# Kernel optimization log

Hardware: AMD Instinct MI355X
Metric: run time of the kernel (lower is better)

The kernel has to match this reference:

```python
import math
import jax, jax.numpy as jnp
import numpy as np

DIM = 4096
N_HEADS = 32
N_KV_HEADS = 8
HEAD_DIM = DIM // N_HEADS          # 128
N_REP = N_HEADS // N_KV_HEADS      # 4
B, T = 2, 2048
MAX_SEQ = 2048
ROPE_THETA = 500000.0


def _rope_tables(seq_len, head_dim, theta):
    inv = 1.0 / (theta ** (np.arange(0, head_dim, 2, dtype=np.float32) / head_dim))
    t = np.arange(seq_len, dtype=np.float32)
    ang = np.outer(t, inv)                      # [T, head_dim/2]
    return jnp.asarray(np.cos(ang)), jnp.asarray(np.sin(ang))


def setup_inputs() -> dict:
    key = jax.random.key(0)
    ks = jax.random.split(key, 6)
    scale = 0.02
    x = jax.random.normal(ks[0], (B, T, DIM), dtype=jnp.float32)
    wq = jax.random.normal(ks[1], (N_HEADS * HEAD_DIM, DIM), dtype=jnp.float32) * scale
    wk = jax.random.normal(ks[2], (N_KV_HEADS * HEAD_DIM, DIM), dtype=jnp.float32) * scale
    wv = jax.random.normal(ks[3], (N_KV_HEADS * HEAD_DIM, DIM), dtype=jnp.float32) * scale
    wo = jax.random.normal(ks[4], (DIM, N_HEADS * HEAD_DIM), dtype=jnp.float32) * scale
    freqs_cos, freqs_sin = _rope_tables(T, HEAD_DIM, ROPE_THETA)
    cache_k = jnp.zeros((B, MAX_SEQ, N_KV_HEADS, HEAD_DIM), dtype=jnp.float32)
    cache_v = jnp.zeros((B, MAX_SEQ, N_KV_HEADS, HEAD_DIM), dtype=jnp.float32)
    mask = jnp.zeros((T, T), dtype=jnp.float32)  # NOTE: unused by the original forward
    return {"x": x, "wq": wq, "wk": wk, "wv": wv, "wo": wo,
            "freqs_cos": freqs_cos, "freqs_sin": freqs_sin,
            "cache_k": cache_k, "cache_v": cache_v,
            "mask": mask, "start_pos": 0}


def _apply_rope(t, cos, sin):
    # t: [B, T, H, hd]; even/odd interleaved pairs form complex numbers
    tr = t.reshape(*t.shape[:-1], HEAD_DIM // 2, 2)
    xr, xi = tr[..., 0], tr[..., 1]
    c = cos[None, :, None, :]
    s = sin[None, :, None, :]
    out_r = xr * c - xi * s
    out_i = xr * s + xi * c
    return jnp.stack([out_r, out_i], axis=-1).reshape(t.shape)


def reference(x, wq, wk, wv, wo, freqs_cos, freqs_sin, cache_k, cache_v, mask, start_pos):
    Bx, Tx, _ = x.shape
    q = (x @ wq.T).reshape(Bx, Tx, N_HEADS, HEAD_DIM)
    k = (x @ wk.T).reshape(Bx, Tx, N_KV_HEADS, HEAD_DIM)
    v = (x @ wv.T).reshape(Bx, Tx, N_KV_HEADS, HEAD_DIM)

    q = _apply_rope(q, freqs_cos, freqs_sin)
    k = _apply_rope(k, freqs_cos, freqs_sin)

    # KV-cache append (start_pos is a static Python int)
    cache_k = jax.lax.dynamic_update_slice(cache_k, k, (0, start_pos, 0, 0))
    cache_v = jax.lax.dynamic_update_slice(cache_v, v, (0, start_pos, 0, 0))
    S = start_pos + Tx

    # GQA expansion via torch-style .repeat (tiling: head h -> kv head h % n_kv)
    keys = jnp.tile(cache_k[:, :S], (1, 1, N_REP, 1))    # [B, S, H, hd]
    values = jnp.tile(cache_v[:, :S], (1, 1, N_REP, 1))  # [B, S, H, hd]

    scores = jnp.einsum('bthd,bshd->bhts', q, keys) / math.sqrt(HEAD_DIM)
    # NOTE: the original forward never adds `mask` — faithful unmasked softmax
    probs = jax.nn.softmax(scores, axis=-1)
    ctx = jnp.einsum('bhts,bshd->bthd', probs, values).reshape(Bx, Tx, N_HEADS * HEAD_DIM)
    return ctx @ wo.T
```

## Files before the change

### kernel.cpp

```cpp
#include <hip/hip_runtime.h>
#include <hip/hip_bf16.h>
#include <cstdint>


typedef short bf16x8 __attribute__((ext_vector_type(8)));
typedef float f32x4  __attribute__((ext_vector_type(4)));

__device__ __forceinline__ float b2f(unsigned short h) {
  union { uint32_t u; float f; } v; v.u = ((uint32_t)h) << 16; return v.f;
}
__device__ __forceinline__ unsigned short f2b(float f) {
  union { float f; uint32_t u; } v; v.f = f;
  uint32_t r = (v.u + 0x7FFFu + ((v.u >> 16) & 1u)) >> 16;
  return (unsigned short)r;
}

#define GLDS16(gp, lp)                                                        \
  __builtin_amdgcn_global_load_lds(                                           \
      (const __attribute__((address_space(1))) unsigned int*)(gp),            \
      (__attribute__((address_space(3))) unsigned int*)(lp), 16, 0, 0)

__global__ __launch_bounds__(256) void cast_f32_bf16(
    const float* __restrict__ in, unsigned short* __restrict__ out, int n4) {
  int i = blockIdx.x * 256 + threadIdx.x;
  if (i < n4) {
    float4 v = ((const float4*)in)[i];
    ushort4 o;
    o.x = f2b(v.x); o.y = f2b(v.y); o.z = f2b(v.z); o.w = f2b(v.w);
    ((ushort4*)out)[i] = o;
  }
}

__device__ __forceinline__ void stout(float* p, float v) { *p = v; }
__device__ __forceinline__ void stout(unsigned short* p, float v) { *p = f2b(v); }

template <typename OUT>
__global__ __launch_bounds__(256, 2) void gemm_bt(
    const unsigned short* __restrict__ A, const unsigned short* __restrict__ B,
    OUT* __restrict__ C, int M, int N, int K) {
  __shared__ __align__(16) unsigned short As[128][64];
  __shared__ __align__(16) unsigned short Bs[128][64];

  const int tid  = threadIdx.x;
  const int lane = tid & 63;
  const int wave = tid >> 6;
  const int col  = lane & 15;
  const int quad = lane >> 4;
  const int bm = blockIdx.y * 128;
  const int bn = blockIdx.x * 128;
  const int wm = (wave & 1) * 64;
  const int wn = (wave >> 1) * 64;

  f32x4 acc[4][4];
#pragma unroll
  for (int i = 0; i < 4; ++i)
#pragma unroll
    for (int j = 0; j < 4; ++j) acc[i][j] = (f32x4){0.f, 0.f, 0.f, 0.f};

  const int srow0  = tid >> 3;
  const int gchunk = (tid & 7) ^ ((tid >> 3) & 7);
  const unsigned short* Ag = A + (size_t)(bm + srow0) * K + gchunk * 8;
  const unsigned short* Bg = B + (size_t)(bn + srow0) * K + gchunk * 8;
  unsigned short* Al = &As[0][0] + tid * 8;
  unsigned short* Bl = &Bs[0][0] + tid * 8;

  for (int k0 = 0; k0 < K; k0 += 64) {
    __syncthreads();
#pragma unroll
    for (int r = 0; r < 4; ++r) {
      GLDS16(Ag + k0 + (size_t)r * 32 * K, Al + r * 2048);
      GLDS16(Bg + k0 + (size_t)r * 32 * K, Bl + r * 2048);
    }
    __syncthreads();
#pragma unroll
    for (int ks = 0; ks < 2; ++ks) {
      bf16x8 a[4], b[4];
      const int slot = ((ks * 4 + quad) ^ (col & 7)) * 8;
#pragma unroll
      for (int i = 0; i < 4; ++i)
        a[i] = *(const bf16x8*)&As[wm + i * 16 + col][slot];
#pragma unroll
      for (int j = 0; j < 4; ++j)
        b[j] = *(const bf16x8*)&Bs[wn + j * 16 + col][slot];
#pragma unroll
      for (int i = 0; i < 4; ++i)
#pragma unroll
        for (int j = 0; j < 4; ++j)
          acc[i][j] = __builtin_amdgcn_mfma_f32_16x16x32_bf16(a[i], b[j],
                                                              acc[i][j], 0, 0, 0);
    }
  }

#pragma unroll
  for (int i = 0; i < 4; ++i) {
    int row = bm + wm + i * 16 + quad * 4;
#pragma unroll
    for (int j = 0; j < 4; ++j) {
      int cc = bn + wn + j * 16 + col;
#pragma unroll
      for (int r2 = 0; r2 < 4; ++r2)
        stout(C + (size_t)(row + r2) * N + cc, acc[i][j][r2]);
    }
  }
}

__global__ __launch_bounds__(256) void rope_qk(
    unsigned short* __restrict__ qkv, const float* __restrict__ cosT,
    const float* __restrict__ sinT) {
  int idx = blockIdx.x * 256 + threadIdx.x;
  int m = idx / 2560;
  int p = idx - m * 2560;
  int head = p >> 6, i = p & 63;
  int t = m & 2047;
  unsigned short* ptr = qkv + (size_t)m * 6144 + head * 128 + i * 2;
  ushort2 xy = *(const ushort2*)ptr;
  float x = b2f(xy.x), y = b2f(xy.y);
  float c = cosT[t * 64 + i], s = sinT[t * 64 + i];
  ushort2 o;
  o.x = f2b(x * c - y * s);
  o.y = f2b(x * s + y * c);
  *(ushort2*)ptr = o;
}

__global__ __launch_bounds__(256) void transpose_v(
    const unsigned short* __restrict__ qkv, unsigned short* __restrict__ vt) {
  __shared__ unsigned short tile[64][72];
  int b = blockIdx.z >> 3, kvh = blockIdx.z & 7;
  int s0 = blockIdx.x * 64, d0 = blockIdx.y * 64;
  int tc = threadIdx.x & 63, tr = threadIdx.x >> 6;
#pragma unroll
  for (int r = 0; r < 16; ++r) {
    int row = r * 4 + tr;
    tile[row][tc] =
        qkv[(size_t)(b * 2048 + s0 + row) * 6144 + 5120 + kvh * 128 + d0 + tc];
  }
  __syncthreads();
#pragma unroll
  for (int r = 0; r < 16; ++r) {
    int drow = r * 4 + tr;
    vt[(size_t)((b * 8 + kvh) * 128 + d0 + drow) * 2048 + s0 + tc] =
        tile[tc][drow];
  }
}

__global__ __launch_bounds__(256, 2) void attn(
    const unsigned short* __restrict__ qkv, const unsigned short* __restrict__ vt,
    unsigned short* __restrict__ ctx) {
  constexpr int T = 2048, LD = 6144;
  const int qt = blockIdx.x, h = blockIdx.y, b = blockIdx.z;
  const int kvh = h & 7;
  const int tid = threadIdx.x, lane = tid & 63, wave = tid >> 6;
  const int col = lane & 15, quad = lane >> 4;

  __shared__ __align__(1024) char smem[49152];
  auto Qs = (unsigned short(*)[128][8])smem;
  auto Ks = (unsigned short(*)[64][8])smem;
  auto Vs = (unsigned short(*)[128][8])(smem + 16384);
  auto Ps = (unsigned short(*)[128][8])(smem + 32768);

  {
    const int row = tid & 127, kc0 = tid >> 7;
    const unsigned short* g =
        qkv + (size_t)(b * T + qt * 128 + row) * LD + h * 128 + kc0 * 8;
    unsigned short* l = &Qs[kc0][row][0];
#pragma unroll
    for (int r = 0; r < 8; ++r) GLDS16(g + r * 16, l + r * 2048);
  }
  __syncthreads();

  bf16x8 qf[2][4];
#pragma unroll
  for (int mi = 0; mi < 2; ++mi)
#pragma unroll
    for (int ks = 0; ks < 4; ++ks)
      qf[mi][ks] = *(const bf16x8*)&Qs[ks * 4 + quad][wave * 32 + mi * 16 + col][0];

  float mrow[2][4], lrow[2][4];
  f32x4 oacc[2][8];
#pragma unroll
  for (int mi = 0; mi < 2; ++mi)
#pragma unroll
    for (int r = 0; r < 4; ++r) { mrow[mi][r] = -1e30f; lrow[mi][r] = 0.f; }
#pragma unroll
  for (int mi = 0; mi < 2; ++mi)
#pragma unroll
    for (int d = 0; d < 8; ++d) oacc[mi][d] = (f32x4){0.f, 0.f, 0.f, 0.f};

  const float scale = 0.08838834764831845f;
  const float l2e = 1.4426950408889634f;

  for (int s0 = 0; s0 < T; s0 += 64) {
    __syncthreads();
    {
      const int srow = tid & 63, kc0 = tid >> 6;
      const unsigned short* g =
          qkv + (size_t)(b * T + s0 + srow) * LD + 4096 + kvh * 128 + kc0 * 8;
      unsigned short* l = &Ks[kc0][srow][0];
#pragma unroll
      for (int r = 0; r < 4; ++r) GLDS16(g + r * 32, l + r * 2048);
      const int drow = tid & 127, sc0 = tid >> 7;
      const unsigned short* gv =
          vt + (size_t)((b * 8 + kvh) * 128 + drow) * T + s0 + sc0 * 8;
      unsigned short* lv = &Vs[sc0][drow][0];
#pragma unroll
      for (int r = 0; r < 4; ++r) GLDS16(gv + r * 16, lv + r * 2048);
    }
    __syncthreads();

    f32x4 sacc[2][4];
#pragma unroll
    for (int mi = 0; mi < 2; ++mi)
#pragma unroll
      for (int j = 0; j < 4; ++j) sacc[mi][j] = (f32x4){0.f, 0.f, 0.f, 0.f};
#pragma unroll
    for (int ks = 0; ks < 4; ++ks) {
      bf16x8 bk[4];
#pragma unroll
      for (int j = 0; j < 4; ++j)
        bk[j] = *(const bf16x8*)&Ks[ks * 4 + quad][j * 16 + col][0];
#pragma unroll
      for (int mi = 0; mi < 2; ++mi)
#pragma unroll
        for (int j = 0; j < 4; ++j)
          sacc[mi][j] = __builtin_amdgcn_mfma_f32_16x16x32_bf16(
              qf[mi][ks], bk[j], sacc[mi][j], 0, 0, 0);
    }

#pragma unroll
    for (int mi = 0; mi < 2; ++mi) {
#pragma unroll
      for (int r = 0; r < 4; ++r) {
        float mx = sacc[mi][0][r];
#pragma unroll
        for (int j = 1; j < 4; ++j) mx = fmaxf(mx, sacc[mi][j][r]);
        mx = fmaxf(mx, __shfl_xor(mx, 1));
        mx = fmaxf(mx, __shfl_xor(mx, 2));
        mx = fmaxf(mx, __shfl_xor(mx, 4));
        mx = fmaxf(mx, __shfl_xor(mx, 8));
        mx *= scale;
        float mold = mrow[mi][r];
        float mnew = fmaxf(mold, mx);
        float alpha = exp2f((mold - mnew) * l2e);
        mrow[mi][r] = mnew;
        float rsum = 0.f;
#pragma unroll
        for (int j = 0; j < 4; ++j) {
          float pv = exp2f((sacc[mi][j][r] * scale - mnew) * l2e);
          sacc[mi][j][r] = pv;
          rsum += pv;
        }
        rsum += __shfl_xor(rsum, 1);
        rsum += __shfl_xor(rsum, 2);
        rsum += __shfl_xor(rsum, 4);
        rsum += __shfl_xor(rsum, 8);
        lrow[mi][r] = lrow[mi][r] * alpha + rsum;
#pragma unroll
        for (int d = 0; d < 8; ++d) oacc[mi][d][r] *= alpha;
        int prow = wave * 32 + mi * 16 + quad * 4 + r;
#pragma unroll
        for (int j = 0; j < 4; ++j) {
          int sc = (j * 16 + col) >> 3;
          Ps[sc][prow][col & 7] = f2b(sacc[mi][j][r]);
        }
      }
    }

#pragma unroll
    for (int ks = 0; ks < 2; ++ks) {
      bf16x8 ap[2];
#pragma unroll
      for (int mi = 0; mi < 2; ++mi)
        ap[mi] = *(const bf16x8*)&Ps[ks * 4 + quad][wave * 32 + mi * 16 + col][0];
#pragma unroll
      for (int di = 0; di < 8; ++di) {
        bf16x8 bv = *(const bf16x8*)&Vs[ks * 4 + quad][di * 16 + col][0];
#pragma unroll
        for (int mi = 0; mi < 2; ++mi)
          oacc[mi][di] = __builtin_amdgcn_mfma_f32_16x16x32_bf16(
              ap[mi], bv, oacc[mi][di], 0, 0, 0);
      }
    }
  }

#pragma unroll
  for (int mi = 0; mi < 2; ++mi) {
#pragma unroll
    for (int r = 0; r < 4; ++r) {
      float inv = 1.0f / lrow[mi][r];
      int row = qt * 128 + wave * 32 + mi * 16 + quad * 4 + r;
#pragma unroll
      for (int di = 0; di < 8; ++di)
        ctx[(size_t)(b * T + row) * 4096 + h * 128 + di * 16 + col] =
            f2b(oacc[mi][di][r] * inv);
    }
  }
}

extern "C" void kernel_launch(void* const* d_in, const int* in_sizes, int n_in,
                              void* d_out, int out_size, void* d_ws,
                              size_t ws_size, hipStream_t stream) {
  const float* x  = (const float*)d_in[0];
  const float* wq = (const float*)d_in[1];
  const float* wk = (const float*)d_in[2];
  const float* wv = (const float*)d_in[3];
  const float* wo = (const float*)d_in[4];
  const float* fc = (const float*)d_in[5];
  const float* fs = (const float*)d_in[6];
  float* out = (float*)d_out;

  char* ws = (char*)d_ws;
  unsigned short* xb  = (unsigned short*)(ws);
  unsigned short* wb  = (unsigned short*)(ws + 33554432);
  unsigned short* qkv = (unsigned short*)(ws + 33554432 + 50331648);
  unsigned short* vtp = (unsigned short*)(ws + 33554432 + 50331648 + 50331648);

  cast_f32_bf16<<<16384, 256, 0, stream>>>(x, xb, 4194304);
  cast_f32_bf16<<<16384, 256, 0, stream>>>(wq, wb, 4194304);
  cast_f32_bf16<<<4096, 256, 0, stream>>>(wk, wb + 16777216, 1048576);
  cast_f32_bf16<<<4096, 256, 0, stream>>>(wv, wb + 20971520, 1048576);

  dim3 g1(48, 32);
  gemm_bt<unsigned short><<<g1, 256, 0, stream>>>(xb, wb, qkv, 4096, 6144, 4096);

  cast_f32_bf16<<<16384, 256, 0, stream>>>(wo, wb, 4194304);

  rope_qk<<<40960, 256, 0, stream>>>(qkv, fc, fs);

  dim3 g2(32, 2, 16);
  transpose_v<<<g2, 256, 0, stream>>>(qkv, vtp);

  dim3 g3(16, 32, 2);
  attn<<<g3, 256, 0, stream>>>(qkv, vtp, xb);

  dim3 g4(32, 32);
  gemm_bt<float><<<g4, 256, 0, stream>>>(xb, wb, out, 4096, 4096, 4096);
}
```

Before: 929.7 us.

## Transpose attention MFMAs so query rows live per lane, with swizzled K/V LDS

The QK^T and PV MFMAs now take K/V as the A operand and Q/P as B, so each lane holds one query's scores across its accumulator registers. The row max and row sum then need only two cross-quad shuffles instead of four per row, and P is written to LDS as packed 4-element vectors. K and V tiles are stored row-major with an XOR swizzle on 16-byte chunks to avoid LDS bank conflicts, and the P buffer is padded to 72 columns. Shared memory grows slightly, which may affect occupancy at two blocks per CU, and the output stores become scattered 2-byte writes.

```diff
diff --git a/kernel.cpp b/kernel.cpp
--- a/kernel.cpp
+++ b/kernel.cpp
@@ -152,11 +152,11 @@
   const int tid = threadIdx.x, lane = tid & 63, wave = tid >> 6;
   const int col = lane & 15, quad = lane >> 4;
 
-  __shared__ __align__(1024) char smem[49152];
+  __shared__ __align__(1024) char smem[51200];
   auto Qs = (unsigned short(*)[128][8])smem;
-  auto Ks = (unsigned short(*)[64][8])smem;
-  auto Vs = (unsigned short(*)[128][8])(smem + 16384);
-  auto Ps = (unsigned short(*)[128][8])(smem + 32768);
+  auto Ks = (unsigned short(*)[128])smem;
+  auto Vs = (unsigned short(*)[64])(smem + 16384);
+  auto Ps = (unsigned short(*)[72])(smem + 32768);
 
   {
     const int row = tid & 127, kc0 = tid >> 7;
@@ -175,12 +175,10 @@
     for (int ks = 0; ks < 4; ++ks)
       qf[mi][ks] = *(const bf16x8*)&Qs[ks * 4 + quad][wave * 32 + mi * 16 + col][0];
 
-  float mrow[2][4], lrow[2][4];
+  float mrow[2], lrow[2];
   f32x4 oacc[2][8];
 #pragma unroll
-  for (int mi = 0; mi < 2; ++mi)
-#pragma unroll
-    for (int r = 0; r < 4; ++r) { mrow[mi][r] = -1e30f; lrow[mi][r] = 0.f; }
+  for (int mi = 0; mi < 2; ++mi) { mrow[mi] = -1e30f; lrow[mi] = 0.f; }
 #pragma unroll
   for (int mi = 0; mi < 2; ++mi)
 #pragma unroll
@@ -188,22 +186,27 @@
 
   const float scale = 0.08838834764831845f;
   const float l2e = 1.4426950408889634f;
+
+  const int krow0 = tid >> 4;
+  const int kgch  = (tid & 15) ^ ((tid >> 4) & 15);
+  const int vrow0 = tid >> 3;
+  const int vgch  = (tid & 7) ^ ((tid >> 3) & 7);
+  unsigned short* Klin = &Ks[0][0] + tid * 8;
+  unsigned short* Vlin = &Vs[0][0] + tid * 8;
 
   for (int s0 = 0; s0 < T; s0 += 64) {
     __syncthreads();
     {
-      const int srow = tid & 63, kc0 = tid >> 6;
       const unsigned short* g =
-          qkv + (size_t)(b * T + s0 + srow) * LD + 4096 + kvh * 128 + kc0 * 8;
-      unsigned short* l = &Ks[kc0][srow][0];
-#pragma unroll
-      for (int r = 0; r < 4; ++r) GLDS16(g + r * 32, l + r * 2048);
-      const int drow = tid & 127, sc0 = tid >> 7;
+          qkv + (size_t)(b * T + s0 + krow0) * LD + 4096 + kvh * 128 + kgch * 8;
+#pragma unroll
+      for (int r = 0; r < 4; ++r)
+        GLDS16(g + (size_t)r * 16 * LD, Klin + r * 2048);
       const unsigned short* gv =
-          vt + (size_t)((b * 8 + kvh) * 128 + drow) * T + s0 + sc0 * 8;
-      unsigned short* lv = &Vs[sc0][drow][0];
-#pragma unroll
-      for (int r = 0; r < 4; ++r) GLDS16(gv + r * 16, lv + r * 2048);
+          vt + (size_t)((b * 8 + kvh) * 128 + vrow0) * T + s0 + vgch * 8;
+#pragma unroll
+      for (int r = 0; r < 4; ++r)
+        GLDS16(gv + (size_t)r * 32 * T, Vlin + r * 2048);
     }
     __syncthreads();
 
@@ -214,85 +217,84 @@
       for (int j = 0; j < 4; ++j) sacc[mi][j] = (f32x4){0.f, 0.f, 0.f, 0.f};
 #pragma unroll
     for (int ks = 0; ks < 4; ++ks) {
-      bf16x8 bk[4];
+      bf16x8 ak[4];
 #pragma unroll
       for (int j = 0; j < 4; ++j)
-        bk[j] = *(const bf16x8*)&Ks[ks * 4 + quad][j * 16 + col][0];
+        ak[j] = *(const bf16x8*)&Ks[j * 16 + col][((ks * 4 + quad) ^ col) * 8];
 #pragma unroll
       for (int mi = 0; mi < 2; ++mi)
 #pragma unroll
         for (int j = 0; j < 4; ++j)
           sacc[mi][j] = __builtin_amdgcn_mfma_f32_16x16x32_bf16(
-              qf[mi][ks], bk[j], sacc[mi][j], 0, 0, 0);
+              ak[j], qf[mi][ks], sacc[mi][j], 0, 0, 0);
     }
 
 #pragma unroll
     for (int mi = 0; mi < 2; ++mi) {
-#pragma unroll
-      for (int r = 0; r < 4; ++r) {
-        float mx = sacc[mi][0][r];
-#pragma unroll
-        for (int j = 1; j < 4; ++j) mx = fmaxf(mx, sacc[mi][j][r]);
-        mx = fmaxf(mx, __shfl_xor(mx, 1));
-        mx = fmaxf(mx, __shfl_xor(mx, 2));
-        mx = fmaxf(mx, __shfl_xor(mx, 4));
-        mx = fmaxf(mx, __shfl_xor(mx, 8));
-        mx *= scale;
-        float mold = mrow[mi][r];
-        float mnew = fmaxf(mold, mx);
-        float alpha = exp2f((mold - mnew) * l2e);
-        mrow[mi][r] = mnew;
-        float rsum = 0.f;
-#pragma unroll
-        for (int j = 0; j < 4; ++j) {
+      const int q = wave * 32 + mi * 16 + col;
+      float mx = sacc[mi][0][0];
+#pragma unroll
+      for (int j = 0; j < 4; ++j)
+#pragma unroll
+        for (int r = 0; r < 4; ++r) mx = fmaxf(mx, sacc[mi][j][r]);
+      mx = fmaxf(mx, __shfl_xor(mx, 16));
+      mx = fmaxf(mx, __shfl_xor(mx, 32));
+      mx *= scale;
+      float mold = mrow[mi];
+      float mnew = fmaxf(mold, mx);
+      float alpha = exp2f((mold - mnew) * l2e);
+      mrow[mi] = mnew;
+      float rsum = 0.f;
+#pragma unroll
+      for (int j = 0; j < 4; ++j) {
+        ushort4 pk;
+#pragma unroll
+        for (int r = 0; r < 4; ++r) {
           float pv = exp2f((sacc[mi][j][r] * scale - mnew) * l2e);
-          sacc[mi][j][r] = pv;
           rsum += pv;
+          ((unsigned short*)&pk)[r] = f2b(pv);
         }
-        rsum += __shfl_xor(rsum, 1);
-        rsum += __shfl_xor(rsum, 2);
-        rsum += __shfl_xor(rsum, 4);
-        rsum += __shfl_xor(rsum, 8);
-        lrow[mi][r] = lrow[mi][r] * alpha + rsum;
-#pragma unroll
-        for (int d = 0; d < 8; ++d) oacc[mi][d][r] *= alpha;
-        int prow = wave * 32 + mi * 16 + quad * 4 + r;
-#pragma unroll
-        for (int j = 0; j < 4; ++j) {
-          int sc = (j * 16 + col) >> 3;
-          Ps[sc][prow][col & 7] = f2b(sacc[mi][j][r]);
+        *(ushort4*)&Ps[q][j * 16 + quad * 4] = pk;
+      }
+      rsum += __shfl_xor(rsum, 16);
+      rsum += __shfl_xor(rsum, 32);
+      lrow[mi] = lrow[mi] * alpha + rsum;
+#pragma unroll
+      for (int di = 0; di < 8; ++di) {
+#pragma unroll
+        for (int r = 0; r < 4; ++r) oacc[mi][di][r] *= alpha;
+      }
+    }
+
+#pragma unroll
+    for (int mi = 0; mi < 2; ++mi) {
+      const int q = wave * 32 + mi * 16 + col;
+      bf16x8 bp[2];
+      bp[0] = *(const bf16x8*)&Ps[q][quad * 8];
+      bp[1] = *(const bf16x8*)&Ps[q][32 + quad * 8];
+#pragma unroll
+      for (int ks = 0; ks < 2; ++ks) {
+#pragma unroll
+        for (int di = 0; di < 8; ++di) {
+          bf16x8 va = *(const bf16x8*)
+              &Vs[di * 16 + col][(((ks * 4 + quad) ^ (col & 7))) * 8];
+          oacc[mi][di] = __builtin_amdgcn_mfma_f32_16x16x32_bf16(
+              va, bp[ks], oacc[mi][di], 0, 0, 0);
         }
       }
     }
-
-#pragma unroll
-    for (int ks = 0; ks < 2; ++ks) {
-      bf16x8 ap[2];
-#pragma unroll
-      for (int mi = 0; mi < 2; ++mi)
-        ap[mi] = *(const bf16x8*)&Ps[ks * 4 + quad][wave * 32 + mi * 16 + col][0];
-#pragma unroll
-      for (int di = 0; di < 8; ++di) {
-        bf16x8 bv = *(const bf16x8*)&Vs[ks * 4 + quad][di * 16 + col][0];
-#pragma unroll
-        for (int mi = 0; mi < 2; ++mi)
-          oacc[mi][di] = __builtin_amdgcn_mfma_f32_16x16x32_bf16(
-              ap[mi], bv, oacc[mi][di], 0, 0, 0);
-      }
-    }
   }
 
 #pragma unroll
   for (int mi = 0; mi < 2; ++mi) {
-#pragma unroll
-    for (int r = 0; r < 4; ++r) {
-      float inv = 1.0f / lrow[mi][r];
-      int row = qt * 128 + wave * 32 + mi * 16 + quad * 4 + r;
-#pragma unroll
-      for (int di = 0; di < 8; ++di)
-        ctx[(size_t)(b * T + row) * 4096 + h * 128 + di * 16 + col] =
-            f2b(oacc[mi][di][r] * inv);
-    }
+    float inv = 1.0f / lrow[mi];
+    int row = qt * 128 + wave * 32 + mi * 16 + col;
+    unsigned short* cp = ctx + (size_t)(b * T + row) * 4096 + h * 128;
+#pragma unroll
+    for (int di = 0; di < 8; ++di)
+#pragma unroll
+      for (int r = 0; r < 4; ++r)
+        cp[di * 16 + quad * 4 + r] = f2b(oacc[mi][di][r] * inv);
   }
 }
 
```

Result: faster. 813.2 us (-12.5%).
